# Performance work log

Measured on AMD Instinct MI355X. Metric: run time of the kernel, lower is better.

The kernel has to match this reference:

```python
import jax, jax.numpy as jnp
import numpy as np

N_QUBITS = 5
N_LAYERS = 3
DIM = 2 ** N_QUBITS  # 32


def _apply_ry(state, theta, w):
    # state: [B, 32] complex64; theta: scalar or [B] float32
    half = theta * 0.5
    c = jnp.cos(half)
    s = jnp.sin(half)
    if c.ndim:  # per-sample angles
        c = c[:, None, None]
        s = s[:, None, None]
    pre, post = 2 ** w, 2 ** (N_QUBITS - 1 - w)
    st = state.reshape(-1, pre, 2, post)
    s0, s1 = st[:, :, 0, :], st[:, :, 1, :]
    out = jnp.stack([c * s0 - s * s1, s * s0 + c * s1], axis=2)
    return out.reshape(-1, DIM)


def _apply_rz(state, theta, w):
    half = theta * 0.5
    e0 = jnp.exp(-1j * half)
    e1 = jnp.exp(1j * half)
    pre, post = 2 ** w, 2 ** (N_QUBITS - 1 - w)
    st = state.reshape(-1, pre, 2, post)
    out = jnp.stack([e0 * st[:, :, 0, :], e1 * st[:, :, 1, :]], axis=2)
    return out.reshape(-1, DIM)


def _apply_cnot(state, c):
    # control wire c, target wire c+1 (adjacent, as in the CNOT chain)
    pre, post = 2 ** c, 2 ** (N_QUBITS - 2 - c)
    st = state.reshape(-1, pre, 2, 2, post)
    out = jnp.stack([st[:, :, 0], st[:, :, 1, ::-1, :]], axis=2)
    return out.reshape(-1, DIM)


def _expval_z(state, w):
    pre, post = 2 ** w, 2 ** (N_QUBITS - 1 - w)
    p = jnp.abs(state.reshape(-1, pre, 2, post)) ** 2
    return (p[:, :, 0, :] - p[:, :, 1, :]).sum(axis=(1, 2))


def _circuit(enc, qp):
    # enc: [B, 5] in [-1,1]; qp: [30]
    B = enc.shape[0]
    state = jnp.zeros((B, DIM), jnp.complex64).at[:, 0].set(1.0)
    pi = jnp.float32(np.pi)
    for i in range(N_QUBITS):
        state = _apply_ry(state, enc[:, i] * pi, i)
    idx = 0
    for _ in range(N_LAYERS):
        for i in range(N_QUBITS):
            state = _apply_ry(state, qp[idx], i); idx += 1
            state = _apply_rz(state, qp[idx], i); idx += 1
        for i in range(N_QUBITS - 1):
            state = _apply_cnot(state, i)
    return jnp.stack([_expval_z(state, i) for i in range(N_QUBITS)], axis=1)


def setup_inputs() -> dict:
    key = jax.random.key(0)
    ks = jax.random.split(key, 14)
    B, S, A = 131072, 252, 4
    def lin(k, fin, fout):
        return jax.random.normal(k, (fin, fout), jnp.float32) / jnp.sqrt(jnp.float32(fin))
    return {
        'state': jax.random.normal(ks[0], (B, S), jnp.float32),
        'W1': lin(ks[1], S, 128), 'b1': jnp.zeros((128,), jnp.float32),
        'W2': lin(ks[2], 128, 64), 'b2': jnp.zeros((64,), jnp.float32),
        'W3': lin(ks[3], 64, N_QUBITS), 'b3': jnp.zeros((N_QUBITS,), jnp.float32),
        'qp': jax.random.normal(ks[4], (N_LAYERS * N_QUBITS * 2,), jnp.float32) * 0.1,
        'D1': lin(ks[5], N_QUBITS, 32), 'd1': jnp.zeros((32,), jnp.float32),
        'D2': lin(ks[6], 32, 16), 'd2': jnp.zeros((16,), jnp.float32),
        'D3': lin(ks[7], 16, A), 'd3': jnp.zeros((A,), jnp.float32),
    }


def reference(state, W1, b1, W2, b2, W3, b3, qp, D1, d1, D2, d2, D3, d3):
    h = jax.nn.relu(state @ W1 + b1)
    h = jax.nn.relu(h @ W2 + b2)
    enc = jnp.tanh(h @ W3 + b3)          # [B, 5]
    q = _circuit(enc, qp)                # [B, 5] PauliZ expectations
    h = jax.nn.relu(q @ D1 + d1)
    h = jax.nn.relu(h @ D2 + d2)
    return h @ D3 + d3                   # [B, action_dim]
```

## Files before the change

### kernel.cpp

```cpp
#include <hip/hip_runtime.h>
#include <hip/hip_bf16.h>
#include <math.h>

typedef _Float16 half8_t __attribute__((ext_vector_type(8)));
typedef _Float16 half4_t __attribute__((ext_vector_type(4)));
typedef float floatx4 __attribute__((ext_vector_type(4)));

#define TPT 8

__device__ __forceinline__ void lds_barrier() {
    asm volatile("s_waitcnt lgkmcnt(0)" ::: "memory");
    __builtin_amdgcn_s_barrier();
    asm volatile("" ::: "memory");
}

__device__ __forceinline__ float fast_tanh(float x) {
    float e = __expf(2.f * x);
    return 1.f - 2.f / (e + 1.f);
}

__device__ __forceinline__ void prep_body(const float* __restrict__ W,
                                          _Float16* __restrict__ dst,
                                          int K, int N, int KS, int b) {
    int ks   = b % KS;
    int nt   = b / KS;
    int lane = threadIdx.x;
    int col  = nt * 16 + (lane & 15);
    int kbase = ks * 32 + ((lane >> 4) << 3);
    half8_t v;
#pragma unroll
    for (int j = 0; j < 8; ++j) {
        int k = kbase + j;
        float x = (k < K && col < N) ? W[(size_t)k * N + col] : 0.f;
        v[j] = (_Float16)x;
    }
    *(half8_t*)(dst + (size_t)(b * 64 + lane) * 8) = v;
}

__global__ void prep_all(const float* __restrict__ W1, const float* __restrict__ W2,
                         const float* __restrict__ W3,
                         _Float16* __restrict__ w1f, _Float16* __restrict__ w2f,
                         _Float16* __restrict__ w3f) {
    int b = blockIdx.x;
    if (b < 64)      prep_body(W1, w1f, 252, 128, 8, b);
    else if (b < 80) prep_body(W2, w2f, 128, 64, 4, b - 64);
    else             prep_body(W3, w3f, 64, 5, 2, b - 80);
}

__global__ __launch_bounds__(512, 4) void front_kernel(
    const float* __restrict__ state,
    const _Float16* __restrict__ w1f, const float* __restrict__ b1,
    const _Float16* __restrict__ w2f, const float* __restrict__ b2,
    const _Float16* __restrict__ w3f, const float* __restrict__ b3,
    float* __restrict__ enc, int Btot) {
    __shared__ char lds[47104];
    const int tid = threadIdx.x;
    const int w   = tid >> 6;
    const int l   = tid & 63;
    const int l15 = l & 15;
    const int lhi = l >> 4;
    const int row0 = blockIdx.x * (32 * TPT);

    const int srow = tid >> 4;
    const int sc0  = tid & 15;
    const int sswz = (srow & 7) << 4;

    floatx4 pf[4];

#define ISSUE_A(T)                                                          \
    {                                                                       \
        const float* Ar = state + (size_t)(row0 + (T) * 32 + srow) * 252;   \
        _Pragma("unroll")                                                   \
        for (int jj = 0; jj < 4; ++jj) {                                    \
            int c = sc0 + jj * 16;                                          \
            if (c < 63) pf[jj] = *(const floatx4*)(Ar + c * 4);             \
        }                                                                   \
    }

    ISSUE_A(0)

    half8_t bw1[8];
#pragma unroll
    for (int ks = 0; ks < 8; ++ks)
        bw1[ks] = *(const half8_t*)(w1f + (size_t)((w * 8 + ks) * 64 + l) * 8);

    {
        const floatx4* s2 = (const floatx4*)w2f;
        *(floatx4*)(lds + 28672 + tid * 16)        = s2[tid];
        *(floatx4*)(lds + 28672 + 8192 + tid * 16) = s2[512 + tid];
        if (tid < 128) {
            const floatx4* s3 = (const floatx4*)w3f;
            *(floatx4*)(lds + 45056 + tid * 16) = s3[tid];
        }
    }

    const float bb1 = b1[w * 16 + l15];
    const float bb2 = b2[(w & 3) * 16 + l15];
    const float bb3 = b3[l15 < 5 ? l15 : 4];

    const int mi2 = w >> 2;
    const int nt2 = w & 3;

#pragma unroll 1
    for (int t = 0; t < TPT; ++t) {
#pragma unroll
        for (int jj = 0; jj < 4; ++jj) {
            int c = sc0 + jj * 16;
            half4_t h;
            if (c == 63) {
                h = half4_t{0, 0, 0, 0};
            } else {
                floatx4 f = pf[jj];
                h = half4_t{ (_Float16)f[0], (_Float16)f[1], (_Float16)f[2], (_Float16)f[3] };
            }
            *(half4_t*)(lds + (srow << 9) + ((c * 8) ^ sswz)) = h;
        }
        if (t + 1 < TPT) ISSUE_A(t + 1)
        lds_barrier();

        floatx4 acc1[2] = { floatx4{0, 0, 0, 0}, floatx4{0, 0, 0, 0} };
#pragma unroll
        for (int ks = 0; ks < 8; ++ks) {
            int cb = ks * 64 + lhi * 16;
#pragma unroll
            for (int mi = 0; mi < 2; ++mi) {
                int r = mi * 16 + l15;
                half8_t a = *(const half8_t*)(lds + (r << 9) + (cb ^ ((r & 7) << 4)));
                acc1[mi] = __builtin_amdgcn_mfma_f32_16x16x32_f16(a, bw1[ks], acc1[mi], 0, 0, 0);
            }
        }

        {
            int col2 = (w * 16 + l15) * 2;
#pragma unroll
            for (int mi = 0; mi < 2; ++mi)
#pragma unroll
                for (int ri = 0; ri < 4; ++ri) {
                    int row = mi * 16 + lhi * 4 + ri;
                    float v = acc1[mi][ri] + bb1;
                    v = v > 0.f ? v : 0.f;
                    *(_Float16*)(lds + 16384 + (row << 8) + (col2 ^ ((row & 7) << 4))) = (_Float16)v;
                }
        }
        lds_barrier();

        floatx4 acc2 = floatx4{0, 0, 0, 0};
#pragma unroll
        for (int ks = 0; ks < 4; ++ks) {
            int r = mi2 * 16 + l15;
            int cb = ks * 64 + lhi * 16;
            half8_t a  = *(const half8_t*)(lds + 16384 + (r << 8) + (cb ^ ((r & 7) << 4)));
            half8_t bf = *(const half8_t*)(lds + 28672 + ((nt2 * 4 + ks) * 64 + l) * 16);
            acc2 = __builtin_amdgcn_mfma_f32_16x16x32_f16(a, bf, acc2, 0, 0, 0);
        }

        {
            int col2 = (nt2 * 16 + l15) * 2;
#pragma unroll
            for (int ri = 0; ri < 4; ++ri) {
                int row = mi2 * 16 + lhi * 4 + ri;
                float v = acc2[ri] + bb2;
                v = v > 0.f ? v : 0.f;
                *(_Float16*)(lds + 24576 + (row << 7) + (col2 ^ ((row & 7) << 4))) = (_Float16)v;
            }
        }
        lds_barrier();

        if (w < 2) {
            floatx4 acc3 = floatx4{0, 0, 0, 0};
#pragma unroll
            for (int ks = 0; ks < 2; ++ks) {
                int r = w * 16 + l15;
                int cb = ks * 64 + lhi * 16;
                half8_t a  = *(const half8_t*)(lds + 24576 + (r << 7) + (cb ^ ((r & 7) << 4)));
                half8_t bf = *(const half8_t*)(lds + 45056 + (ks * 64 + l) * 16);
                acc3 = __builtin_amdgcn_mfma_f32_16x16x32_f16(a, bf, acc3, 0, 0, 0);
            }
            if (l15 < 5) {
#pragma unroll
                for (int ri = 0; ri < 4; ++ri) {
                    int grow = row0 + t * 32 + w * 16 + lhi * 4 + ri;
                    enc[(size_t)l15 * Btot + grow] = fast_tanh(acc3[ri] + bb3);
                }
            }
        }
    }
#undef ISSUE_A
}

template<int P>
__device__ __forceinline__ void ry_g(float* re, float* im, float c, float s) {
    constexpr int STR = 1 << P;
#pragma unroll
    for (int base = 0; base < 32; base += 2 * STR)
#pragma unroll
        for (int d = 0; d < STR; ++d) {
            int i0 = base + d, i1 = i0 + STR;
            float r0 = re[i0], r1 = re[i1], m0 = im[i0], m1 = im[i1];
            re[i0] = c * r0 - s * r1;  re[i1] = s * r0 + c * r1;
            im[i0] = c * m0 - s * m1;  im[i1] = s * m0 + c * m1;
        }
}

template<int P>
__device__ __forceinline__ void rz_g(float* re, float* im, float c, float s) {
#pragma unroll
    for (int i = 0; i < 32; ++i) {
        float t = ((i >> P) & 1) ? s : -s;
        float r = re[i], m = im[i];
        re[i] = c * r - t * m;
        im[i] = c * m + t * r;
    }
}

template<int PC, int PT>
__device__ __forceinline__ void cnot_g(float* re, float* im) {
#pragma unroll
    for (int i = 0; i < 32; ++i) {
        if (((i >> PC) & 1) && !((i >> PT) & 1)) {
            int j = i | (1 << PT);
            float t;
            t = re[i]; re[i] = re[j]; re[j] = t;
            t = im[i]; im[i] = im[j]; im[j] = t;
        }
    }
}

__global__ __launch_bounds__(256) void back_kernel(
    const float* __restrict__ enc, const float* __restrict__ qp,
    const float* __restrict__ D1, const float* __restrict__ d1,
    const float* __restrict__ D2, const float* __restrict__ d2,
    const float* __restrict__ D3, const float* __restrict__ d3,
    float* __restrict__ out, int Btot) {
    __shared__ float sD1[160], sd1[32], sD2[512], sd2[16], sD3[64], sd3[4];
    __shared__ float sQc[30], sQs[30];
    const int tid = threadIdx.x;
    for (int i = tid; i < 512; i += 256) sD2[i] = D2[i];
    if (tid < 160) sD1[tid] = D1[tid];
    if (tid < 32)  sd1[tid] = d1[tid];
    if (tid < 64)  sD3[tid] = D3[tid];
    if (tid < 16)  sd2[tid] = d2[tid];
    if (tid < 4)   sd3[tid] = d3[tid];
    if (tid < 30) { float h = 0.5f * qp[tid]; sQc[tid] = cosf(h); sQs[tid] = sinf(h); }
    __syncthreads();

    const size_t r = (size_t)blockIdx.x * 256 + tid;

    float cq[5], sq[5];
    const float HPI = 1.57079632679489662f;
#pragma unroll
    for (int i = 0; i < 5; ++i) {
        float a = enc[(size_t)i * Btot + r] * HPI;
        cq[i] = __cosf(a);
        sq[i] = __sinf(a);
    }
    float re[32], im[32];
#pragma unroll
    for (int i = 0; i < 32; ++i) {
        float v = ((i >> 4) & 1) ? sq[0] : cq[0];
        v *= ((i >> 3) & 1) ? sq[1] : cq[1];
        v *= ((i >> 2) & 1) ? sq[2] : cq[2];
        v *= ((i >> 1) & 1) ? sq[3] : cq[3];
        v *= ( i       & 1) ? sq[4] : cq[4];
        re[i] = v;
        im[i] = 0.f;
    }

#pragma unroll
    for (int lay = 0; lay < 3; ++lay) {
        const float* c = sQc + lay * 10;
        const float* s = sQs + lay * 10;
        ry_g<4>(re, im, c[0], s[0]);  rz_g<4>(re, im, c[1], s[1]);
        ry_g<3>(re, im, c[2], s[2]);  rz_g<3>(re, im, c[3], s[3]);
        ry_g<2>(re, im, c[4], s[4]);  rz_g<2>(re, im, c[5], s[5]);
        ry_g<1>(re, im, c[6], s[6]);  rz_g<1>(re, im, c[7], s[7]);
        ry_g<0>(re, im, c[8], s[8]);  rz_g<0>(re, im, c[9], s[9]);
        cnot_g<4, 3>(re, im);
        cnot_g<3, 2>(re, im);
        cnot_g<2, 1>(re, im);
        cnot_g<1, 0>(re, im);
    }

    float q[5] = {0, 0, 0, 0, 0};
#pragma unroll
    for (int i = 0; i < 32; ++i) {
        float p = re[i] * re[i] + im[i] * im[i];
        q[0] += ((i >> 4) & 1) ? -p : p;
        q[1] += ((i >> 3) & 1) ? -p : p;
        q[2] += ((i >> 2) & 1) ? -p : p;
        q[3] += ((i >> 1) & 1) ? -p : p;
        q[4] += ( i       & 1) ? -p : p;
    }

    float h1[32];
#pragma unroll
    for (int j = 0; j < 32; ++j) {
        float a = sd1[j];
#pragma unroll
        for (int k = 0; k < 5; ++k) a += q[k] * sD1[k * 32 + j];
        h1[j] = a > 0.f ? a : 0.f;
    }
    float h2[16];
#pragma unroll
    for (int j = 0; j < 16; ++j) {
        float a = sd2[j];
#pragma unroll
        for (int k = 0; k < 32; ++k) a += h1[k] * sD2[k * 16 + j];
        h2[j] = a > 0.f ? a : 0.f;
    }
    floatx4 o;
#pragma unroll
    for (int j = 0; j < 4; ++j) {
        float a = sd3[j];
#pragma unroll
        for (int k = 0; k < 16; ++k) a += h2[k] * sD3[k * 4 + j];
        o[j] = a;
    }
    *(floatx4*)(out + r * 4) = o;
}

extern "C" void kernel_launch(void* const* d_in, const int* in_sizes, int n_in,
                              void* d_out, int out_size, void* d_ws, size_t ws_size,
                              hipStream_t stream) {
    const float* state = (const float*)d_in[0];
    const float* W1 = (const float*)d_in[1];
    const float* b1 = (const float*)d_in[2];
    const float* W2 = (const float*)d_in[3];
    const float* b2 = (const float*)d_in[4];
    const float* W3 = (const float*)d_in[5];
    const float* b3 = (const float*)d_in[6];
    const float* qp = (const float*)d_in[7];
    const float* D1 = (const float*)d_in[8];
    const float* d1 = (const float*)d_in[9];
    const float* D2 = (const float*)d_in[10];
    const float* d2 = (const float*)d_in[11];
    const float* D3 = (const float*)d_in[12];
    const float* d3 = (const float*)d_in[13];
    float* out = (float*)d_out;

    const int B = in_sizes[0] / 252;

    char* ws = (char*)d_ws;
    _Float16* w1f = (_Float16*)ws;
    _Float16* w2f = (_Float16*)(ws + 65536);
    _Float16* w3f = (_Float16*)(ws + 65536 + 16384);
    float*    enc = (float*)(ws + 65536 + 16384 + 2048);

    prep_all<<<82, 64, 0, stream>>>(W1, W2, W3, w1f, w2f, w3f);
    front_kernel<<<B / (32 * TPT), 512, 0, stream>>>(state, w1f, b1, w2f, b2, w3f, b3, enc, B);
    back_kernel<<<B / 256, 256, 0, stream>>>(enc, qp, D1, d1, D2, d2, D3, d3, out, B);
}
```

Baseline: 55.78 us.

## Double-buffer A tile in front kernel and fold first circuit layer analytically

The front kernel now double-buffers the staged input tile in LDS and defers the layer-3 MFMA/tanh of each tile to the next iteration. This removes one barrier per tile and overlaps the fp16 conversion and staging of tile t+1 with the layer-2 work of tile t. The back kernel folds the encoding RY and the first layer's RY/RZ gates into a per-qubit product state, since RY composes by adding angles and RZ is diagonal, so one of three gate layers is removed. The cost is more LDS per block, which may reduce occupancy, and qp trig now uses fast intrinsics with slightly lower precision.

```diff
diff --git a/kernel.cpp b/kernel.cpp
--- a/kernel.cpp
+++ b/kernel.cpp
@@ -53,7 +53,7 @@
     const _Float16* __restrict__ w2f, const float* __restrict__ b2,
     const _Float16* __restrict__ w3f, const float* __restrict__ b3,
     float* __restrict__ enc, int Btot) {
-    __shared__ char lds[47104];
+    __shared__ char lds[63488];
     const int tid = threadIdx.x;
     const int w   = tid >> 6;
     const int l   = tid & 63;
@@ -77,6 +77,24 @@
         }                                                                   \
     }
 
+#define STAGE(T)                                                            \
+    {                                                                       \
+        int sab = (((T) & 1) << 14);                                        \
+        _Pragma("unroll")                                                   \
+        for (int jj = 0; jj < 4; ++jj) {                                    \
+            int c = sc0 + jj * 16;                                          \
+            half4_t h;                                                      \
+            if (c == 63) {                                                  \
+                h = half4_t{0, 0, 0, 0};                                    \
+            } else {                                                        \
+                floatx4 f = pf[jj];                                         \
+                h = half4_t{ (_Float16)f[0], (_Float16)f[1],                \
+                             (_Float16)f[2], (_Float16)f[3] };              \
+            }                                                               \
+            *(half4_t*)(lds + sab + (srow << 9) + ((c * 8) ^ sswz)) = h;    \
+        }                                                                   \
+    }
+
     ISSUE_A(0)
 
     half8_t bw1[8];
@@ -86,11 +104,11 @@
 
     {
         const floatx4* s2 = (const floatx4*)w2f;
-        *(floatx4*)(lds + 28672 + tid * 16)        = s2[tid];
-        *(floatx4*)(lds + 28672 + 8192 + tid * 16) = s2[512 + tid];
+        *(floatx4*)(lds + 45056 + tid * 16)        = s2[tid];
+        *(floatx4*)(lds + 45056 + 8192 + tid * 16) = s2[512 + tid];
         if (tid < 128) {
             const floatx4* s3 = (const floatx4*)w3f;
-            *(floatx4*)(lds + 45056 + tid * 16) = s3[tid];
+            *(floatx4*)(lds + 61440 + tid * 16) = s3[tid];
         }
     }
 
@@ -101,23 +119,32 @@
     const int mi2 = w >> 2;
     const int nt2 = w & 3;
 
-#pragma unroll 1
+    STAGE(0)
+    ISSUE_A(1)
+    lds_barrier();
+
+#pragma unroll
     for (int t = 0; t < TPT; ++t) {
-#pragma unroll
-        for (int jj = 0; jj < 4; ++jj) {
-            int c = sc0 + jj * 16;
-            half4_t h;
-            if (c == 63) {
-                h = half4_t{0, 0, 0, 0};
-            } else {
-                floatx4 f = pf[jj];
-                h = half4_t{ (_Float16)f[0], (_Float16)f[1], (_Float16)f[2], (_Float16)f[3] };
+        if (w < 2 && t > 0) {
+            floatx4 acc3 = floatx4{0, 0, 0, 0};
+#pragma unroll
+            for (int ks = 0; ks < 2; ++ks) {
+                int r = w * 16 + l15;
+                int cb = ks * 64 + lhi * 16;
+                half8_t a  = *(const half8_t*)(lds + 40960 + (r << 7) + (cb ^ ((r & 7) << 4)));
+                half8_t bf = *(const half8_t*)(lds + 61440 + (ks * 64 + l) * 16);
+                acc3 = __builtin_amdgcn_mfma_f32_16x16x32_f16(a, bf, acc3, 0, 0, 0);
             }
-            *(half4_t*)(lds + (srow << 9) + ((c * 8) ^ sswz)) = h;
-        }
-        if (t + 1 < TPT) ISSUE_A(t + 1)
-        lds_barrier();
-
+            if (l15 < 5) {
+#pragma unroll
+                for (int ri = 0; ri < 4; ++ri) {
+                    int grow = row0 + (t - 1) * 32 + w * 16 + lhi * 4 + ri;
+                    enc[(size_t)l15 * Btot + grow] = fast_tanh(acc3[ri] + bb3);
+                }
+            }
+        }
+
+        const int sab = (t & 1) << 14;
         floatx4 acc1[2] = { floatx4{0, 0, 0, 0}, floatx4{0, 0, 0, 0} };
 #pragma unroll
         for (int ks = 0; ks < 8; ++ks) {
@@ -125,7 +152,7 @@
 #pragma unroll
             for (int mi = 0; mi < 2; ++mi) {
                 int r = mi * 16 + l15;
-                half8_t a = *(const half8_t*)(lds + (r << 9) + (cb ^ ((r & 7) << 4)));
+                half8_t a = *(const half8_t*)(lds + sab + (r << 9) + (cb ^ ((r & 7) << 4)));
                 acc1[mi] = __builtin_amdgcn_mfma_f32_16x16x32_f16(a, bw1[ks], acc1[mi], 0, 0, 0);
             }
         }
@@ -139,7 +166,7 @@
                     int row = mi * 16 + lhi * 4 + ri;
                     float v = acc1[mi][ri] + bb1;
                     v = v > 0.f ? v : 0.f;
-                    *(_Float16*)(lds + 16384 + (row << 8) + (col2 ^ ((row & 7) << 4))) = (_Float16)v;
+                    *(_Float16*)(lds + 32768 + (row << 8) + (col2 ^ ((row & 7) << 4))) = (_Float16)v;
                 }
         }
         lds_barrier();
@@ -149,8 +176,8 @@
         for (int ks = 0; ks < 4; ++ks) {
             int r = mi2 * 16 + l15;
             int cb = ks * 64 + lhi * 16;
-            half8_t a  = *(const half8_t*)(lds + 16384 + (r << 8) + (cb ^ ((r & 7) << 4)));
-            half8_t bf = *(const half8_t*)(lds + 28672 + ((nt2 * 4 + ks) * 64 + l) * 16);
+            half8_t a  = *(const half8_t*)(lds + 32768 + (r << 8) + (cb ^ ((r & 7) << 4)));
+            half8_t bf = *(const half8_t*)(lds + 45056 + ((nt2 * 4 + ks) * 64 + l) * 16);
             acc2 = __builtin_amdgcn_mfma_f32_16x16x32_f16(a, bf, acc2, 0, 0, 0);
         }
 
@@ -161,31 +188,37 @@
                 int row = mi2 * 16 + lhi * 4 + ri;
                 float v = acc2[ri] + bb2;
                 v = v > 0.f ? v : 0.f;
-                *(_Float16*)(lds + 24576 + (row << 7) + (col2 ^ ((row & 7) << 4))) = (_Float16)v;
+                *(_Float16*)(lds + 40960 + (row << 7) + (col2 ^ ((row & 7) << 4))) = (_Float16)v;
             }
         }
+
+        if (t + 1 < TPT) {
+            STAGE(t + 1)
+            if (t + 2 < TPT) ISSUE_A(t + 2)
+        }
         lds_barrier();
-
-        if (w < 2) {
-            floatx4 acc3 = floatx4{0, 0, 0, 0};
-#pragma unroll
-            for (int ks = 0; ks < 2; ++ks) {
-                int r = w * 16 + l15;
-                int cb = ks * 64 + lhi * 16;
-                half8_t a  = *(const half8_t*)(lds + 24576 + (r << 7) + (cb ^ ((r & 7) << 4)));
-                half8_t bf = *(const half8_t*)(lds + 45056 + (ks * 64 + l) * 16);
-                acc3 = __builtin_amdgcn_mfma_f32_16x16x32_f16(a, bf, acc3, 0, 0, 0);
+    }
+
+    if (w < 2) {
+        floatx4 acc3 = floatx4{0, 0, 0, 0};
+#pragma unroll
+        for (int ks = 0; ks < 2; ++ks) {
+            int r = w * 16 + l15;
+            int cb = ks * 64 + lhi * 16;
+            half8_t a  = *(const half8_t*)(lds + 40960 + (r << 7) + (cb ^ ((r & 7) << 4)));
+            half8_t bf = *(const half8_t*)(lds + 61440 + (ks * 64 + l) * 16);
+            acc3 = __builtin_amdgcn_mfma_f32_16x16x32_f16(a, bf, acc3, 0, 0, 0);
+        }
+        if (l15 < 5) {
+#pragma unroll
+            for (int ri = 0; ri < 4; ++ri) {
+                int grow = row0 + (TPT - 1) * 32 + w * 16 + lhi * 4 + ri;
+                enc[(size_t)l15 * Btot + grow] = fast_tanh(acc3[ri] + bb3);
             }
-            if (l15 < 5) {
-#pragma unroll
-                for (int ri = 0; ri < 4; ++ri) {
-                    int grow = row0 + t * 32 + w * 16 + lhi * 4 + ri;
-                    enc[(size_t)l15 * Btot + grow] = fast_tanh(acc3[ri] + bb3);
-                }
-            }
         }
     }
 #undef ISSUE_A
+#undef STAGE
 }
 
 template<int P>
@@ -223,6 +256,19 @@
             t = re[i]; re[i] = re[j]; re[j] = t;
             t = im[i]; im[i] = im[j]; im[j] = t;
         }
+    }
+}
+
+template<int P>
+__device__ __forceinline__ void expand_g(float* re, float* im,
+                                         float arv, float aiv, float brv, float biv) {
+#pragma unroll
+    for (int base = 0; base < 32; base += (2 << P)) {
+        float cr = re[base], ci = im[base];
+        re[base + (1 << P)] = cr * brv - ci * biv;
+        im[base + (1 << P)] = cr * biv + ci * brv;
+        re[base] = cr * arv - ci * aiv;
+        im[base] = cr * aiv + ci * arv;
     }
 }
 
@@ -233,7 +279,8 @@
     const float* __restrict__ D3, const float* __restrict__ d3,
     float* __restrict__ out, int Btot) {
     __shared__ float sD1[160], sd1[32], sD2[512], sd2[16], sD3[64], sd3[4];
-    __shared__ float sQc[30], sQs[30];
+    __shared__ float sQc[20], sQs[20];
+    __shared__ float ryh[5], rzc0[5], rzs0[5];
     const int tid = threadIdx.x;
     for (int i = tid; i < 512; i += 256) sD2[i] = D2[i];
     if (tid < 160) sD1[tid] = D1[tid];
@@ -241,33 +288,41 @@
     if (tid < 64)  sD3[tid] = D3[tid];
     if (tid < 16)  sd2[tid] = d2[tid];
     if (tid < 4)   sd3[tid] = d3[tid];
-    if (tid < 30) { float h = 0.5f * qp[tid]; sQc[tid] = cosf(h); sQs[tid] = sinf(h); }
+    if (tid < 20) { float h = 0.5f * qp[10 + tid]; sQc[tid] = __cosf(h); sQs[tid] = __sinf(h); }
+    if (tid < 5) {
+        ryh[tid] = 0.5f * qp[2 * tid];
+        float h = 0.5f * qp[2 * tid + 1];
+        rzc0[tid] = __cosf(h);
+        rzs0[tid] = __sinf(h);
+    }
     __syncthreads();
 
     const size_t r = (size_t)blockIdx.x * 256 + tid;
 
-    float cq[5], sq[5];
     const float HPI = 1.57079632679489662f;
+    float ar[5], ai[5], br[5], bi[5];
 #pragma unroll
     for (int i = 0; i < 5; ++i) {
-        float a = enc[(size_t)i * Btot + r] * HPI;
-        cq[i] = __cosf(a);
-        sq[i] = __sinf(a);
-    }
+        float h = enc[(size_t)i * Btot + r] * HPI + ryh[i];
+        float ch = __cosf(h), sh = __sinf(h);
+        ar[i] = ch * rzc0[i];  ai[i] = -ch * rzs0[i];
+        br[i] = sh * rzc0[i];  bi[i] =  sh * rzs0[i];
+    }
+
     float re[32], im[32];
-#pragma unroll
-    for (int i = 0; i < 32; ++i) {
-        float v = ((i >> 4) & 1) ? sq[0] : cq[0];
-        v *= ((i >> 3) & 1) ? sq[1] : cq[1];
-        v *= ((i >> 2) & 1) ? sq[2] : cq[2];
-        v *= ((i >> 1) & 1) ? sq[3] : cq[3];
-        v *= ( i       & 1) ? sq[4] : cq[4];
-        re[i] = v;
-        im[i] = 0.f;
-    }
-
-#pragma unroll
-    for (int lay = 0; lay < 3; ++lay) {
+    re[0] = ar[0]; im[0] = ai[0]; re[16] = br[0]; im[16] = bi[0];
+    expand_g<3>(re, im, ar[1], ai[1], br[1], bi[1]);
+    expand_g<2>(re, im, ar[2], ai[2], br[2], bi[2]);
+    expand_g<1>(re, im, ar[3], ai[3], br[3], bi[3]);
+    expand_g<0>(re, im, ar[4], ai[4], br[4], bi[4]);
+
+    cnot_g<4, 3>(re, im);
+    cnot_g<3, 2>(re, im);
+    cnot_g<2, 1>(re, im);
+    cnot_g<1, 0>(re, im);
+
+#pragma unroll
+    for (int lay = 0; lay < 2; ++lay) {
         const float* c = sQc + lay * 10;
         const float* s = sQs + lay * 10;
         ry_g<4>(re, im, c[0], s[0]);  rz_g<4>(re, im, c[1], s[1]);
```

Result: faster. 54.64 us (median of 3 runs) (-2.1%).
